# Kernel tuning notes

Hardware: AMD Instinct MI355X
Metric: run time of the kernel (lower is better)

Reference implementation:

```python
import jax, jax.numpy as jnp
import numpy as np

N = 10000    # base mesh vertices
M = 500000   # extended (target) vertices
B = 128      # batch of scalar fields


def setup_inputs() -> dict:
    key = jax.random.key(0)
    k1, k2, k3 = jax.random.split(key, 3)
    f_values = jax.random.normal(k1, (B, N), dtype=jnp.float32)
    # Each target point lies in one spherical triangle -> 3 vertex indices.
    tri_idx = jax.random.randint(k2, (M, 3), 0, N, dtype=jnp.int32)
    # Barycentric weights are nonnegative and sum to 1 per target point.
    w = jax.random.uniform(k3, (M, 3), dtype=jnp.float32)
    bary_weights = w / jnp.sum(w, axis=1, keepdims=True)
    return {"f_values": f_values, "tri_idx": tri_idx, "bary_weights": bary_weights}


def reference(f_values, tri_idx, bary_weights):
    # Equivalent to f_values @ W where W (N, M) has <=3 nonzeros per column
    # (barycentric weights at the containing triangle's vertices).
    gathered = jnp.take(f_values, tri_idx, axis=-1)          # (..., M, 3)
    return jnp.einsum('...mk,mk->...m', gathered, bary_weights)  # (..., M)
```

## Files before the change

### kernel.cpp

```cpp
#include <hip/hip_runtime.h>

#define NV     10000
#define MPTS   500000
#define BATCH  128

#define BLOCK  1024
#define G      2
#define MBLK   (BLOCK * 4 * G)
#define BPB    32
#define BSPLIT (BATCH / BPB)
#define PAIRS  (BPB / 2)
#define NGROUPS ((MPTS + MBLK - 1) / MBLK)
#define GRID   256

typedef float v4f __attribute__((ext_vector_type(4)));
typedef int   v4i __attribute__((ext_vector_type(4)));

__device__ inline void lds_barrier() {
    asm volatile("s_waitcnt lgkmcnt(0)" ::: "memory");
    __builtin_amdgcn_sched_barrier(0);
    __builtin_amdgcn_s_barrier();
}

__global__ __launch_bounds__(BLOCK, 4)
void bary_interp_kernel(const float* __restrict__ f,
                        const int*   __restrict__ tri,
                        const float* __restrict__ w,
                        float*       __restrict__ out)
{
    __shared__ v4f buf4[2][NV / 2];

    const int bid = (int)blockIdx.x;
    const int xcd = bid & 7;
    const int seq = bid >> 3;
    const int g   = xcd * 8 + (seq >> 2);
    const int y   = seq & 3;
    if (g >= NGROUPS) return;

    const int tid    = (int)threadIdx.x;
    const int m_base = g * MBLK;
    const int b0     = y * BPB;

    int   idx[G][12];
    float wt [G][12];
    bool  valid[G];
#pragma unroll
    for (int gg = 0; gg < G; ++gg) {
        const int m = m_base + gg * (BLOCK * 4) + tid * 4;
        valid[gg] = (m < MPTS);
        if (valid[gg]) {
            const v4i* ti = reinterpret_cast<const v4i*>(tri + 3 * (size_t)m);
            const v4f* wi = reinterpret_cast<const v4f*>(w + 3 * (size_t)m);
#pragma unroll
            for (int q = 0; q < 3; ++q) {
                const v4i a  = ti[q];
                const v4f bv = wi[q];
#pragma unroll
                for (int e = 0; e < 4; ++e) {
                    idx[gg][4*q+e] = a[e];
                    wt [gg][4*q+e] = bv[e];
                }
            }
        } else {
#pragma unroll
            for (int q = 0; q < 12; ++q) { idx[gg][q] = 0; wt[gg][q] = 0.0f; }
        }
    }

    auto stage = [&](v4f* dst, int b) {
        const v4f* fa = reinterpret_cast<const v4f*>(f + (size_t)b * NV);
        const v4f* fb = reinterpret_cast<const v4f*>(f + (size_t)(b + 1) * NV);
        for (int i = tid; i < NV / 4; i += BLOCK) {
            const v4f a = fa[i];
            const v4f c = fb[i];
            v4f lo = { a.x, c.x, a.y, c.y };
            v4f hi = { a.z, c.z, a.w, c.w };
            dst[2*i+0] = lo;
            dst[2*i+1] = hi;
        }
    };

    stage(buf4[0], b0);
    lds_barrier();

    for (int p = 0; p < PAIRS; ++p) {
        if (p + 1 < PAIRS) stage(buf4[(p + 1) & 1], b0 + 2 * (p + 1));

        const float2* row2 = reinterpret_cast<const float2*>(buf4[p & 1]);
        const int b  = b0 + 2 * p;
        float* oa = out + (size_t)b * MPTS;
        float* ob = oa + MPTS;

#pragma unroll
        for (int gg = 0; gg < G; ++gg) {
            if (valid[gg]) {
                const int m = m_base + gg * (BLOCK * 4) + tid * 4;
                v4f ra, rc;
#pragma unroll
                for (int e = 0; e < 4; ++e) {
                    const float2 v0 = row2[idx[gg][3*e+0]];
                    const float2 v1 = row2[idx[gg][3*e+1]];
                    const float2 v2 = row2[idx[gg][3*e+2]];
                    ra[e] = v0.x*wt[gg][3*e+0] + v1.x*wt[gg][3*e+1] + v2.x*wt[gg][3*e+2];
                    rc[e] = v0.y*wt[gg][3*e+0] + v1.y*wt[gg][3*e+1] + v2.y*wt[gg][3*e+2];
                }
                __builtin_nontemporal_store(ra, reinterpret_cast<v4f*>(oa + m));
                __builtin_nontemporal_store(rc, reinterpret_cast<v4f*>(ob + m));
            }
        }
        lds_barrier();
    }
}

extern "C" void kernel_launch(void* const* d_in, const int* in_sizes, int n_in,
                              void* d_out, int out_size, void* d_ws, size_t ws_size,
                              hipStream_t stream) {
    const float* f   = (const float*)d_in[0];
    const int*   tri = (const int*)  d_in[1];
    const float* w   = (const float*)d_in[2];
    float*       out = (float*)d_out;

    bary_interp_kernel<<<dim3(GRID), BLOCK, 0, stream>>>(f, tri, w, out);
}
```

Before: 58.32 us.

## Gather four batch rows per LDS read and prefetch rows through registers

The LDS table now holds four batch rows interleaved per vertex as float4, so each gathered index returns values for four output rows at once. This halves the number of LDS gathers and the number of barrier-separated passes. Double-buffering in LDS is replaced by prefetching the next quad of rows into registers while the current one is computed. The cost is higher register pressure (48 extra floats of prefetch) and a larger single LDS buffer (160KB), which may reduce occupancy.

```diff
diff --git a/kernel.cpp b/kernel.cpp
--- a/kernel.cpp
+++ b/kernel.cpp
@@ -8,10 +8,10 @@
 #define G      2
 #define MBLK   (BLOCK * 4 * G)
 #define BPB    32
-#define BSPLIT (BATCH / BPB)
-#define PAIRS  (BPB / 2)
+#define QUADS  (BPB / 4)
 #define NGROUPS ((MPTS + MBLK - 1) / MBLK)
 #define GRID   256
+#define NQ     (NV / 4)
 
 typedef float v4f __attribute__((ext_vector_type(4)));
 typedef int   v4i __attribute__((ext_vector_type(4)));
@@ -28,7 +28,7 @@
                         const float* __restrict__ w,
                         float*       __restrict__ out)
 {
-    __shared__ v4f buf4[2][NV / 2];
+    __shared__ v4f buf[NV];
 
     const int bid = (int)blockIdx.x;
     const int xcd = bid & 7;
@@ -67,48 +67,76 @@
         }
     }
 
-    auto stage = [&](v4f* dst, int b) {
-        const v4f* fa = reinterpret_cast<const v4f*>(f + (size_t)b * NV);
+    v4f pa[3], pb[3], pc[3], pd[3];
+
+    auto load_quad = [&](int b) {
+        const v4f* fa = reinterpret_cast<const v4f*>(f + (size_t)(b + 0) * NV);
         const v4f* fb = reinterpret_cast<const v4f*>(f + (size_t)(b + 1) * NV);
-        for (int i = tid; i < NV / 4; i += BLOCK) {
-            const v4f a = fa[i];
-            const v4f c = fb[i];
-            v4f lo = { a.x, c.x, a.y, c.y };
-            v4f hi = { a.z, c.z, a.w, c.w };
-            dst[2*i+0] = lo;
-            dst[2*i+1] = hi;
+        const v4f* fc = reinterpret_cast<const v4f*>(f + (size_t)(b + 2) * NV);
+        const v4f* fd = reinterpret_cast<const v4f*>(f + (size_t)(b + 3) * NV);
+#pragma unroll
+        for (int j = 0; j < 3; ++j) {
+            const int i = tid + j * BLOCK;
+            if (i < NQ) { pa[j] = fa[i]; pb[j] = fb[i]; pc[j] = fc[i]; pd[j] = fd[i]; }
         }
     };
 
-    stage(buf4[0], b0);
-    lds_barrier();
+    auto write_quad = [&]() {
+#pragma unroll
+        for (int j = 0; j < 3; ++j) {
+            const int i = tid + j * BLOCK;
+            if (i < NQ) {
+                v4f t0 = { pa[j].x, pb[j].x, pc[j].x, pd[j].x };
+                v4f t1 = { pa[j].y, pb[j].y, pc[j].y, pd[j].y };
+                v4f t2 = { pa[j].z, pb[j].z, pc[j].z, pd[j].z };
+                v4f t3 = { pa[j].w, pb[j].w, pc[j].w, pd[j].w };
+                buf[4*i+0] = t0;
+                buf[4*i+1] = t1;
+                buf[4*i+2] = t2;
+                buf[4*i+3] = t3;
+            }
+        }
+    };
 
-    for (int p = 0; p < PAIRS; ++p) {
-        if (p + 1 < PAIRS) stage(buf4[(p + 1) & 1], b0 + 2 * (p + 1));
+    load_quad(b0);
 
-        const float2* row2 = reinterpret_cast<const float2*>(buf4[p & 1]);
-        const int b  = b0 + 2 * p;
-        float* oa = out + (size_t)b * MPTS;
-        float* ob = oa + MPTS;
+    for (int p = 0; p < QUADS; ++p) {
+        const int b = b0 + 4 * p;
+
+        if (p) lds_barrier();
+        write_quad();
+        if (p + 1 < QUADS) load_quad(b0 + 4 * (p + 1));
+        lds_barrier();
+
+        float* o0 = out + (size_t)(b + 0) * MPTS;
+        float* o1 = out + (size_t)(b + 1) * MPTS;
+        float* o2 = out + (size_t)(b + 2) * MPTS;
+        float* o3 = out + (size_t)(b + 3) * MPTS;
 
 #pragma unroll
         for (int gg = 0; gg < G; ++gg) {
             if (valid[gg]) {
                 const int m = m_base + gg * (BLOCK * 4) + tid * 4;
-                v4f ra, rc;
+                v4f s0, s1, s2, s3;
 #pragma unroll
                 for (int e = 0; e < 4; ++e) {
-                    const float2 v0 = row2[idx[gg][3*e+0]];
-                    const float2 v1 = row2[idx[gg][3*e+1]];
-                    const float2 v2 = row2[idx[gg][3*e+2]];
-                    ra[e] = v0.x*wt[gg][3*e+0] + v1.x*wt[gg][3*e+1] + v2.x*wt[gg][3*e+2];
-                    rc[e] = v0.y*wt[gg][3*e+0] + v1.y*wt[gg][3*e+1] + v2.y*wt[gg][3*e+2];
+                    const v4f v0 = buf[idx[gg][3*e+0]];
+                    const v4f v1 = buf[idx[gg][3*e+1]];
+                    const v4f v2 = buf[idx[gg][3*e+2]];
+                    const float w0 = wt[gg][3*e+0];
+                    const float w1 = wt[gg][3*e+1];
+                    const float w2 = wt[gg][3*e+2];
+                    s0[e] = v0.x*w0 + v1.x*w1 + v2.x*w2;
+                    s1[e] = v0.y*w0 + v1.y*w1 + v2.y*w2;
+                    s2[e] = v0.z*w0 + v1.z*w1 + v2.z*w2;
+                    s3[e] = v0.w*w0 + v1.w*w1 + v2.w*w2;
                 }
-                __builtin_nontemporal_store(ra, reinterpret_cast<v4f*>(oa + m));
-                __builtin_nontemporal_store(rc, reinterpret_cast<v4f*>(ob + m));
+                __builtin_nontemporal_store(s0, reinterpret_cast<v4f*>(o0 + m));
+                __builtin_nontemporal_store(s1, reinterpret_cast<v4f*>(o1 + m));
+                __builtin_nontemporal_store(s2, reinterpret_cast<v4f*>(o2 + m));
+                __builtin_nontemporal_store(s3, reinterpret_cast<v4f*>(o3 + m));
             }
         }
-        lds_barrier();
     }
 }
 
```

After: 80.56 us. +38.1%, slower.
